# Performance work log

Hardware: AMD Instinct MI355X
Metric: run time of the kernel (lower is better)

Reference implementation:

```python
import jax, jax.numpy as jnp
import numpy as np

QUEST_DIM = 768
C, X, Y = 2048, 19, 19
B = 64

def setup_inputs() -> dict:
    key = jax.random.key(0)
    k1, k2, k3, k4 = jax.random.split(key, 4)
    text_fts = jax.random.normal(k1, (B, QUEST_DIM), dtype=jnp.float32)
    img_fts = jax.random.normal(k2, (B, C, X, Y), dtype=jnp.float32)
    # Linear params (PyTorch nn.Linear: y = x @ W.T + b)
    bound = 1.0 / np.sqrt(QUEST_DIM)
    W = jax.random.uniform(k3, (C, QUEST_DIM), minval=-bound, maxval=bound, dtype=jnp.float32)
    b = jax.random.uniform(k4, (C,), minval=-bound, maxval=bound, dtype=jnp.float32)
    return {"text_fts": text_fts, "img_fts": img_fts, "W": W, "b": b}

def reference(text_fts, img_fts, W, b):
    batch = text_fts.shape[0]
    q = text_fts @ W.T + b                      # [B, C]
    img_flat = img_fts.reshape(batch, C, X * Y) # [B, C, S]
    sims = jnp.einsum('bc,bcs->bs', q, img_flat)  # dot over channel dim
    weights = jax.nn.softmax(sims, axis=1)        # softmax over spatial locations
    final_ans = jnp.einsum('bcs,bs->bc', img_flat, weights)  # weighted pooling
    return final_ans
```

## Files before the change

### kernel.cpp

```cpp
#include <hip/hip_runtime.h>
#include <math.h>

#define Bsz  64
#define Cch  2048
#define Kdim 768
#define Ssp  361
#define CPB  16
#define REGF (CPB * Ssp)
#define NFULL 22
#define NTAIL 36

__device__ __forceinline__ void dma16(const float* g, float* l) {
    __builtin_amdgcn_global_load_lds(
        (const __attribute__((address_space(1))) void*)(g),
        (__attribute__((address_space(3))) void*)(l),
        16, 0, 0);
}

__device__ __forceinline__ void stage_slice(const float* region, float* lds,
                                            int wv, int lane) {
    for (int i = wv; i < NFULL + 1; i += 6) {
        if (i < NFULL || lane < NTAIL)
            dma16(region + i * 256 + lane * 4, lds + i * 256);
    }
    asm volatile("s_waitcnt vmcnt(0)" ::: "memory");
}

__global__ __launch_bounds__(256) void k_qgemm(
    const float* __restrict__ text, const float* __restrict__ W,
    const float* __restrict__ bias, float* __restrict__ qT)
{
    const int lane = threadIdx.x & 63;
    const int wv   = threadIdx.x >> 6;
    const int c0   = blockIdx.x * 8 + wv * 2;
    const int b0   = blockIdx.y * 8;

    const float4* wA = (const float4*)(W + (size_t)c0 * Kdim);
    const float4* wB = (const float4*)(W + (size_t)(c0 + 1) * Kdim);
    const float4 a0 = wA[lane*3+0], a1 = wA[lane*3+1], a2 = wA[lane*3+2];
    const float4 g0 = wB[lane*3+0], g1 = wB[lane*3+1], g2 = wB[lane*3+2];
    const float biasA = bias[c0], biasB = bias[c0 + 1];

    for (int b = b0; b < b0 + 8; b += 2) {
        const float4* tp = (const float4*)(text + (size_t)b * Kdim);
        const float4* up = (const float4*)(text + (size_t)(b + 1) * Kdim);
        const float4 t0 = tp[lane*3+0], t1 = tp[lane*3+1], t2 = tp[lane*3+2];
        const float4 u0 = up[lane*3+0], u1 = up[lane*3+1], u2 = up[lane*3+2];

        float r00 = a0.x*t0.x + a0.y*t0.y + a0.z*t0.z + a0.w*t0.w
                  + a1.x*t1.x + a1.y*t1.y + a1.z*t1.z + a1.w*t1.w
                  + a2.x*t2.x + a2.y*t2.y + a2.z*t2.z + a2.w*t2.w;
        float r10 = g0.x*t0.x + g0.y*t0.y + g0.z*t0.z + g0.w*t0.w
                  + g1.x*t1.x + g1.y*t1.y + g1.z*t1.z + g1.w*t1.w
                  + g2.x*t2.x + g2.y*t2.y + g2.z*t2.z + g2.w*t2.w;
        float r01 = a0.x*u0.x + a0.y*u0.y + a0.z*u0.z + a0.w*u0.w
                  + a1.x*u1.x + a1.y*u1.y + a1.z*u1.z + a1.w*u1.w
                  + a2.x*u2.x + a2.y*u2.y + a2.z*u2.z + a2.w*u2.w;
        float r11 = g0.x*u0.x + g0.y*u0.y + g0.z*u0.z + g0.w*u0.w
                  + g1.x*u1.x + g1.y*u1.y + g1.z*u1.z + g1.w*u1.w
                  + g2.x*u2.x + g2.y*u2.y + g2.z*u2.z + g2.w*u2.w;
        #pragma unroll
        for (int off = 32; off; off >>= 1) {
            r00 += __shfl_xor(r00, off);
            r10 += __shfl_xor(r10, off);
            r01 += __shfl_xor(r01, off);
            r11 += __shfl_xor(r11, off);
        }
        if (lane == 0) {
            qT[(size_t)c0 * Bsz + b]           = r00 + biasA;
            qT[(size_t)(c0 + 1) * Bsz + b]     = r10 + biasB;
            qT[(size_t)c0 * Bsz + b + 1]       = r01 + biasA;
            qT[(size_t)(c0 + 1) * Bsz + b + 1] = r11 + biasB;
        }
    }
}

__global__ __launch_bounds__(384) void k_sims(
    const float* __restrict__ img, const float* __restrict__ qT,
    float* __restrict__ sims_part)
{
    const int b  = blockIdx.x;
    const int cg = blockIdx.y;
    const int tid = threadIdx.x;
    const int lane = tid & 63;
    const int wv   = tid >> 6;

    __shared__ float lds[REGF];
    __shared__ float qL[CPB];

    if (tid < CPB) qL[tid] = qT[(size_t)(cg * CPB + tid) * Bsz + b];

    const float* region = img + ((size_t)b * Cch + (size_t)cg * CPB) * Ssp;
    stage_slice(region, lds, wv, lane);
    __syncthreads();

    if (tid < Ssp) {
        float acc = 0.f;
        #pragma unroll
        for (int c = 0; c < CPB; c++)
            acc += qL[c] * lds[c * Ssp + tid];
        sims_part[((size_t)b * 128 + cg) * Ssp + tid] = acc;
    }
}

__global__ __launch_bounds__(384) void k_wts(
    const float* __restrict__ sims_part, float* __restrict__ wts)
{
    const int b   = blockIdx.x;
    const int tid = threadIdx.x;
    const int lane = tid & 63;
    const int wv   = tid >> 6;

    __shared__ float red[6];

    float s0 = -1e30f;
    if (tid < Ssp) {
        const float* sp = sims_part + (size_t)b * 128 * Ssp + tid;
        float a = 0.f;
        for (int g0 = 0; g0 < 128; g0 += 16) {
            float v[16];
            #pragma unroll
            for (int j = 0; j < 16; j++) v[j] = sp[(size_t)(g0 + j) * Ssp];
            #pragma unroll
            for (int j = 0; j < 16; j++) a += v[j];
        }
        s0 = a;
    }

    float m = s0;
    #pragma unroll
    for (int off = 32; off; off >>= 1) m = fmaxf(m, __shfl_xor(m, off));
    if (lane == 0) red[wv] = m;
    __syncthreads();
    m = red[0];
    #pragma unroll
    for (int w = 1; w < 6; w++) m = fmaxf(m, red[w]);
    __syncthreads();

    const float e0 = (tid < Ssp) ? __expf(s0 - m) : 0.f;
    float l = e0;
    #pragma unroll
    for (int off = 32; off; off >>= 1) l += __shfl_xor(l, off);
    if (lane == 0) red[wv] = l;
    __syncthreads();
    l = red[0] + red[1] + red[2] + red[3] + red[4] + red[5];

    if (tid < Ssp)
        wts[(size_t)b * Ssp + tid] = e0 / l;
}

__global__ __launch_bounds__(384) void k_pool(
    const float* __restrict__ img, const float* __restrict__ wts,
    float* __restrict__ out)
{
    const int b   = blockIdx.x;
    const int cg  = blockIdx.y;
    const int tid = threadIdx.x;
    const int lane = tid & 63;
    const int wv   = tid >> 6;

    __shared__ float lds[REGF];
    __shared__ float wL[Ssp];
    __shared__ float partial[6 * CPB];

    if (tid < Ssp) wL[tid] = wts[(size_t)b * Ssp + tid];

    const float* region = img + ((size_t)b * Cch + (size_t)cg * CPB) * Ssp;
    stage_slice(region, lds, wv, lane);
    __syncthreads();

    const int c    = lane & 15;
    const int sl   = lane >> 4;
    const int s_lo = sl * 90 + (sl > 0 ? 1 : 0);
    const int s_hi = s_lo + (sl > 0 ? 90 : 91);

    float p = 0.f;
    for (int s = s_lo + wv; s < s_hi; s += 6)
        p += lds[c * Ssp + s] * wL[s];

    p += __shfl_xor(p, 16);
    p += __shfl_xor(p, 32);
    if (lane < CPB) partial[wv * CPB + lane] = p;
    __syncthreads();

    if (tid < CPB) {
        float r = partial[tid];
        #pragma unroll
        for (int w = 1; w < 6; w++) r += partial[w * CPB + tid];
        out[(size_t)b * Cch + (size_t)cg * CPB + tid] = r;
    }
}

extern "C" void kernel_launch(void* const* d_in, const int* in_sizes, int n_in,
                              void* d_out, int out_size, void* d_ws, size_t ws_size,
                              hipStream_t stream) {
    const float* text = (const float*)d_in[0];
    const float* img  = (const float*)d_in[1];
    const float* W    = (const float*)d_in[2];
    const float* bias = (const float*)d_in[3];
    float* out = (float*)d_out;

    float* qT        = (float*)d_ws;
    float* sims_part = qT + (size_t)Cch * Bsz;
    float* wts       = sims_part + (size_t)Bsz * 128 * Ssp;

    k_qgemm<<<dim3(256, 8),   256, 0, stream>>>(text, W, bias, qT);
    k_sims <<<dim3(Bsz, 128), 384, 0, stream>>>(img, qT, sims_part);
    k_wts  <<<dim3(Bsz),      384, 0, stream>>>(sims_part, wts);
    k_pool <<<dim3(Bsz, 128), 384, 0, stream>>>(img, wts, out);
}
```

Baseline: 316.7 us.

## Fuse all four stages into one persistent cooperative kernel with grid syncs

Replaces the four separate launches (query GEMM, partial sims, softmax, pooling) with a single cooperative persistent kernel that loops over work items and uses grid-wide syncs between phases. Grid size comes from the occupancy query and is rounded to a multiple of the batch size, so each block keeps one batch row of softmax weights in LDS. This removes kernel launch gaps and tail effects, at the cost of grid barrier overhead and fewer waves per block. If the cooperative launch fails, it falls back to the original four kernels.

```diff
diff --git a/kernel.cpp b/kernel.cpp
--- a/kernel.cpp
+++ b/kernel.cpp
@@ -1,5 +1,8 @@
 #include <hip/hip_runtime.h>
+#include <hip/hip_cooperative_groups.h>
 #include <math.h>
+
+namespace cg = cooperative_groups;
 
 #define Bsz  64
 #define Cch  2048
@@ -9,6 +12,8 @@
 #define REGF (CPB * Ssp)
 #define NFULL 22
 #define NTAIL 36
+#define NCG   (Cch / CPB)
+#define NSLICE (Bsz * NCG)
 
 __device__ __forceinline__ void dma16(const float* g, float* l) {
     __builtin_amdgcn_global_load_lds(
@@ -17,13 +22,179 @@
         16, 0, 0);
 }
 
+template <int NW>
 __device__ __forceinline__ void stage_slice(const float* region, float* lds,
                                             int wv, int lane) {
-    for (int i = wv; i < NFULL + 1; i += 6) {
+    for (int i = wv; i < NFULL + 1; i += NW) {
         if (i < NFULL || lane < NTAIL)
             dma16(region + i * 256 + lane * 4, lds + i * 256);
     }
     asm volatile("s_waitcnt vmcnt(0)" ::: "memory");
+}
+
+__global__ __launch_bounds__(256, 4) void k_fused(
+    const float* __restrict__ text, const float* __restrict__ img,
+    const float* __restrict__ W,    const float* __restrict__ bias,
+    float* __restrict__ qT, float* __restrict__ sims_part,
+    float* __restrict__ wts, float* __restrict__ out)
+{
+    const int tid  = threadIdx.x;
+    const int lane = tid & 63;
+    const int wv   = tid >> 6;
+    const int bid  = blockIdx.x;
+    const int nblk = gridDim.x;
+
+    __shared__ __align__(16) float lds[REGF];
+    __shared__ float aux[Ssp];
+    __shared__ float partial[256];
+
+    cg::grid_group grid = cg::this_grid();
+
+    for (int t = bid * 4 + wv; t < 8192; t += nblk * 4) {
+        const int c0 = (t & 1023) * 2;
+        const int b0 = (t >> 10) * 8;
+        const float4* wA = (const float4*)(W + (size_t)c0 * Kdim);
+        const float4* wB = (const float4*)(W + (size_t)(c0 + 1) * Kdim);
+        const float4 a0 = wA[lane*3+0], a1 = wA[lane*3+1], a2 = wA[lane*3+2];
+        const float4 g0 = wB[lane*3+0], g1 = wB[lane*3+1], g2 = wB[lane*3+2];
+        const float biasA = bias[c0], biasB = bias[c0 + 1];
+
+        for (int b = b0; b < b0 + 8; b += 2) {
+            const float4* tp = (const float4*)(text + (size_t)b * Kdim);
+            const float4* up = (const float4*)(text + (size_t)(b + 1) * Kdim);
+            const float4 t0 = tp[lane*3+0], t1 = tp[lane*3+1], t2 = tp[lane*3+2];
+            const float4 u0 = up[lane*3+0], u1 = up[lane*3+1], u2 = up[lane*3+2];
+
+            float r00 = a0.x*t0.x + a0.y*t0.y + a0.z*t0.z + a0.w*t0.w
+                      + a1.x*t1.x + a1.y*t1.y + a1.z*t1.z + a1.w*t1.w
+                      + a2.x*t2.x + a2.y*t2.y + a2.z*t2.z + a2.w*t2.w;
+            float r10 = g0.x*t0.x + g0.y*t0.y + g0.z*t0.z + g0.w*t0.w
+                      + g1.x*t1.x + g1.y*t1.y + g1.z*t1.z + g1.w*t1.w
+                      + g2.x*t2.x + g2.y*t2.y + g2.z*t2.z + g2.w*t2.w;
+            float r01 = a0.x*u0.x + a0.y*u0.y + a0.z*u0.z + a0.w*u0.w
+                      + a1.x*u1.x + a1.y*u1.y + a1.z*u1.z + a1.w*u1.w
+                      + a2.x*u2.x + a2.y*u2.y + a2.z*u2.z + a2.w*u2.w;
+            float r11 = g0.x*u0.x + g0.y*u0.y + g0.z*u0.z + g0.w*u0.w
+                      + g1.x*u1.x + g1.y*u1.y + g1.z*u1.z + g1.w*u1.w
+                      + g2.x*u2.x + g2.y*u2.y + g2.z*u2.z + g2.w*u2.w;
+            #pragma unroll
+            for (int off = 32; off; off >>= 1) {
+                r00 += __shfl_xor(r00, off);
+                r10 += __shfl_xor(r10, off);
+                r01 += __shfl_xor(r01, off);
+                r11 += __shfl_xor(r11, off);
+            }
+            if (lane == 0) {
+                qT[(size_t)c0 * Bsz + b]           = r00 + biasA;
+                qT[(size_t)(c0 + 1) * Bsz + b]     = r10 + biasB;
+                qT[(size_t)c0 * Bsz + b + 1]       = r01 + biasA;
+                qT[(size_t)(c0 + 1) * Bsz + b + 1] = r11 + biasB;
+            }
+        }
+    }
+
+    __threadfence();
+    grid.sync();
+    __threadfence();
+
+    for (int sl = bid; sl < NSLICE; sl += nblk) {
+        const int b   = sl & (Bsz - 1);
+        const int cgi = sl >> 6;
+        if (tid < CPB)
+            aux[tid] = qT[(size_t)(cgi * CPB + tid) * Bsz + b];
+        const float* region = img + ((size_t)b * Cch + (size_t)cgi * CPB) * Ssp;
+        stage_slice<4>(region, lds, wv, lane);
+        __syncthreads();
+        for (int s = tid; s < Ssp; s += 256) {
+            float acc = 0.f;
+            #pragma unroll
+            for (int c = 0; c < CPB; c++)
+                acc += aux[c] * lds[c * Ssp + s];
+            sims_part[((size_t)b * NCG + cgi) * Ssp + s] = acc;
+        }
+        __syncthreads();
+    }
+
+    __threadfence();
+    grid.sync();
+    __threadfence();
+
+    if (bid < Bsz) {
+        const int b = bid;
+        const float* sp = sims_part + (size_t)b * NCG * Ssp;
+        float sa, sb = -1e30f;
+        {
+            float a = 0.f;
+            for (int g0 = 0; g0 < NCG; g0 += 16) {
+                float v[16];
+                #pragma unroll
+                for (int j = 0; j < 16; j++) v[j] = sp[(size_t)(g0 + j) * Ssp + tid];
+                #pragma unroll
+                for (int j = 0; j < 16; j++) a += v[j];
+            }
+            sa = a;
+        }
+        if (tid < Ssp - 256) {
+            float a = 0.f;
+            for (int g0 = 0; g0 < NCG; g0 += 16) {
+                float v[16];
+                #pragma unroll
+                for (int j = 0; j < 16; j++) v[j] = sp[(size_t)(g0 + j) * Ssp + tid + 256];
+                #pragma unroll
+                for (int j = 0; j < 16; j++) a += v[j];
+            }
+            sb = a;
+        }
+        float m = fmaxf(sa, sb);
+        #pragma unroll
+        for (int off = 32; off; off >>= 1) m = fmaxf(m, __shfl_xor(m, off));
+        if (lane == 0) partial[wv] = m;
+        __syncthreads();
+        m = fmaxf(fmaxf(partial[0], partial[1]), fmaxf(partial[2], partial[3]));
+        __syncthreads();
+        const float ea = __expf(sa - m);
+        const float eb = (tid < Ssp - 256) ? __expf(sb - m) : 0.f;
+        float l = ea + eb;
+        #pragma unroll
+        for (int off = 32; off; off >>= 1) l += __shfl_xor(l, off);
+        if (lane == 0) partial[wv] = l;
+        __syncthreads();
+        l = partial[0] + partial[1] + partial[2] + partial[3];
+        wts[(size_t)b * Ssp + tid] = ea / l;
+        if (tid < Ssp - 256) wts[(size_t)b * Ssp + tid + 256] = eb / l;
+    }
+
+    __threadfence();
+    grid.sync();
+    __threadfence();
+
+    {
+        const int b = bid & (Bsz - 1);
+        for (int s = tid; s < Ssp; s += 256)
+            aux[s] = wts[(size_t)b * Ssp + s];
+    }
+    __syncthreads();
+    for (int sl = bid; sl < NSLICE; sl += nblk) {
+        const int b   = sl & (Bsz - 1);
+        const int cgi = sl >> 6;
+        const float* region = img + ((size_t)b * Cch + (size_t)cgi * CPB) * Ssp;
+        stage_slice<4>(region, lds, wv, lane);
+        __syncthreads();
+        const int c = tid & 15;
+        const int g = tid >> 4;
+        float p = 0.f;
+        for (int s = g; s < Ssp; s += 16)
+            p += lds[c * Ssp + s] * aux[s];
+        partial[tid] = p;
+        __syncthreads();
+        if (tid < CPB) {
+            float r = 0.f;
+            #pragma unroll
+            for (int gg = 0; gg < 16; gg++) r += partial[gg * 16 + tid];
+            out[(size_t)b * Cch + (size_t)cgi * CPB + tid] = r;
+        }
+        __syncthreads();
+    }
 }
 
 __global__ __launch_bounds__(256) void k_qgemm(
@@ -80,7 +251,7 @@
     float* __restrict__ sims_part)
 {
     const int b  = blockIdx.x;
-    const int cg = blockIdx.y;
+    const int cgi = blockIdx.y;
     const int tid = threadIdx.x;
     const int lane = tid & 63;
     const int wv   = tid >> 6;
@@ -88,10 +259,10 @@
     __shared__ float lds[REGF];
     __shared__ float qL[CPB];
 
-    if (tid < CPB) qL[tid] = qT[(size_t)(cg * CPB + tid) * Bsz + b];
-
-    const float* region = img + ((size_t)b * Cch + (size_t)cg * CPB) * Ssp;
-    stage_slice(region, lds, wv, lane);
+    if (tid < CPB) qL[tid] = qT[(size_t)(cgi * CPB + tid) * Bsz + b];
+
+    const float* region = img + ((size_t)b * Cch + (size_t)cgi * CPB) * Ssp;
+    stage_slice<6>(region, lds, wv, lane);
     __syncthreads();
 
     if (tid < Ssp) {
@@ -99,7 +270,7 @@
         #pragma unroll
         for (int c = 0; c < CPB; c++)
             acc += qL[c] * lds[c * Ssp + tid];
-        sims_part[((size_t)b * 128 + cg) * Ssp + tid] = acc;
+        sims_part[((size_t)b * NCG + cgi) * Ssp + tid] = acc;
     }
 }
 
@@ -115,9 +286,9 @@
 
     float s0 = -1e30f;
     if (tid < Ssp) {
-        const float* sp = sims_part + (size_t)b * 128 * Ssp + tid;
+        const float* sp = sims_part + (size_t)b * NCG * Ssp + tid;
         float a = 0.f;
-        for (int g0 = 0; g0 < 128; g0 += 16) {
+        for (int g0 = 0; g0 < NCG; g0 += 16) {
             float v[16];
             #pragma unroll
             for (int j = 0; j < 16; j++) v[j] = sp[(size_t)(g0 + j) * Ssp];
@@ -154,7 +325,7 @@
     float* __restrict__ out)
 {
     const int b   = blockIdx.x;
-    const int cg  = blockIdx.y;
+    const int cgi = blockIdx.y;
     const int tid = threadIdx.x;
     const int lane = tid & 63;
     const int wv   = tid >> 6;
@@ -165,8 +336,8 @@
 
     if (tid < Ssp) wL[tid] = wts[(size_t)b * Ssp + tid];
 
-    const float* region = img + ((size_t)b * Cch + (size_t)cg * CPB) * Ssp;
-    stage_slice(region, lds, wv, lane);
+    const float* region = img + ((size_t)b * Cch + (size_t)cgi * CPB) * Ssp;
+    stage_slice<6>(region, lds, wv, lane);
     __syncthreads();
 
     const int c    = lane & 15;
@@ -187,7 +358,7 @@
         float r = partial[tid];
         #pragma unroll
         for (int w = 1; w < 6; w++) r += partial[w * CPB + tid];
-        out[(size_t)b * Cch + (size_t)cg * CPB + tid] = r;
+        out[(size_t)b * Cch + (size_t)cgi * CPB + tid] = r;
     }
 }
 
@@ -202,10 +373,49 @@
 
     float* qT        = (float*)d_ws;
     float* sims_part = qT + (size_t)Cch * Bsz;
-    float* wts       = sims_part + (size_t)Bsz * 128 * Ssp;
-
-    k_qgemm<<<dim3(256, 8),   256, 0, stream>>>(text, W, bias, qT);
-    k_sims <<<dim3(Bsz, 128), 384, 0, stream>>>(img, qT, sims_part);
-    k_wts  <<<dim3(Bsz),      384, 0, stream>>>(sims_part, wts);
-    k_pool <<<dim3(Bsz, 128), 384, 0, stream>>>(img, wts, out);
-}
+    float* wts       = sims_part + (size_t)Bsz * NCG * Ssp;
+
+    static int mode = 0;
+    static int nblk = 1024;
+    if (mode == 0) {
+        int bpc = 0;
+        if (hipOccupancyMaxActiveBlocksPerMultiprocessor(
+                &bpc, reinterpret_cast<const void*>(&k_fused), 256, 0) != hipSuccess
+            || bpc < 1)
+            bpc = 2;
+        int cus = 256;
+        hipDeviceProp_t prop;
+        int dev = 0;
+        if (hipGetDevice(&dev) == hipSuccess &&
+            hipGetDeviceProperties(&prop, dev) == hipSuccess &&
+            prop.multiProcessorCount > 0)
+            cus = prop.multiProcessorCount;
+        long long nb = (long long)bpc * cus;
+        if (nb > 2048) nb = 2048;
+        nb -= nb % 64;
+        if (nb < 64) nb = 64;
+        nblk = (int)nb;
+        mode = 1;
+    }
+
+    bool done = false;
+    if (mode != 2) {
+        void* args[8] = {(void*)&text, (void*)&img, (void*)&W, (void*)&bias,
+                         (void*)&qT, (void*)&sims_part, (void*)&wts, (void*)&out};
+        hipError_t e = hipLaunchCooperativeKernel(
+            reinterpret_cast<const void*>(&k_fused),
+            dim3(nblk), dim3(256), args, 0, stream);
+        if (e == hipSuccess) {
+            done = true;
+        } else {
+            mode = 2;
+            (void)hipGetLastError();
+        }
+    }
+    if (!done) {
+        k_qgemm<<<dim3(256, 8),   256, 0, stream>>>(text, W, bias, qT);
+        k_sims <<<dim3(Bsz, NCG), 384, 0, stream>>>(img, qT, sims_part);
+        k_wts  <<<dim3(Bsz),      384, 0, stream>>>(sims_part, wts);
+        k_pool <<<dim3(Bsz, NCG), 384, 0, stream>>>(img, wts, out);
+    }
+}
```

After: 711.4 us. 2.25x slower.

## Restructure pooling kernel to read image directly with per-wave channel rows

Applied to the files above, without the earlier changes.

The pooling kernel no longer stages a 16-channel slice into LDS through global_load_lds DMA. Each block now covers 128 channels and each wave covers 32 of them, four rows at a time. Every lane loads spatial elements straight from global memory, multiplies them by weights held in registers, and reduces across the wave with shuffles. This removes the LDS staging, the barrier wait and the cross-wave partial reduction, and cuts the grid from 8192 to 1024 blocks. The cost is lower parallelism, and the row loads are unaligned and coalesced only per row, with a tail that is partly masked.

```diff
diff --git a/kernel.cpp b/kernel.cpp
--- a/kernel.cpp
+++ b/kernel.cpp
@@ -9,6 +9,7 @@
 #define REGF (CPB * Ssp)
 #define NFULL 22
 #define NTAIL 36
+#define NCG   (Cch / CPB)
 
 __device__ __forceinline__ void dma16(const float* g, float* l) {
     __builtin_amdgcn_global_load_lds(
@@ -99,7 +100,7 @@
         #pragma unroll
         for (int c = 0; c < CPB; c++)
             acc += qL[c] * lds[c * Ssp + tid];
-        sims_part[((size_t)b * 128 + cg) * Ssp + tid] = acc;
+        sims_part[((size_t)b * NCG + cg) * Ssp + tid] = acc;
     }
 }
 
@@ -115,7 +116,7 @@
 
     float s0 = -1e30f;
     if (tid < Ssp) {
-        const float* sp = sims_part + (size_t)b * 128 * Ssp + tid;
+        const float* sp = sims_part + (size_t)b * NCG * Ssp + tid;
         float a = 0.f;
         for (int g0 = 0; g0 < 128; g0 += 16) {
             float v[16];
@@ -149,45 +150,62 @@
         wts[(size_t)b * Ssp + tid] = e0 / l;
 }
 
-__global__ __launch_bounds__(384) void k_pool(
+__global__ __launch_bounds__(256) void k_pool(
     const float* __restrict__ img, const float* __restrict__ wts,
     float* __restrict__ out)
 {
-    const int b   = blockIdx.x;
-    const int cg  = blockIdx.y;
-    const int tid = threadIdx.x;
+    const int b    = blockIdx.x;
+    const int cg   = blockIdx.y;
+    const int tid  = threadIdx.x;
     const int lane = tid & 63;
     const int wv   = tid >> 6;
 
-    __shared__ float lds[REGF];
     __shared__ float wL[Ssp];
-    __shared__ float partial[6 * CPB];
-
-    if (tid < Ssp) wL[tid] = wts[(size_t)b * Ssp + tid];
-
-    const float* region = img + ((size_t)b * Cch + (size_t)cg * CPB) * Ssp;
-    stage_slice(region, lds, wv, lane);
-    __syncthreads();
-
-    const int c    = lane & 15;
-    const int sl   = lane >> 4;
-    const int s_lo = sl * 90 + (sl > 0 ? 1 : 0);
-    const int s_hi = s_lo + (sl > 0 ? 90 : 91);
-
-    float p = 0.f;
-    for (int s = s_lo + wv; s < s_hi; s += 6)
-        p += lds[c * Ssp + s] * wL[s];
-
-    p += __shfl_xor(p, 16);
-    p += __shfl_xor(p, 32);
-    if (lane < CPB) partial[wv * CPB + lane] = p;
-    __syncthreads();
-
-    if (tid < CPB) {
-        float r = partial[tid];
-        #pragma unroll
-        for (int w = 1; w < 6; w++) r += partial[w * CPB + tid];
-        out[(size_t)b * Cch + (size_t)cg * CPB + tid] = r;
+    for (int s = tid; s < Ssp; s += 256)
+        wL[s] = wts[(size_t)b * Ssp + s];
+    __syncthreads();
+
+    float wreg[6];
+    #pragma unroll
+    for (int k = 0; k < 6; k++) {
+        const int s = lane + 64 * k;
+        wreg[k] = (s < Ssp) ? wL[s] : 0.f;
+    }
+
+    const float* base = img + ((size_t)b * Cch + (size_t)cg * 128) * Ssp;
+    const int c0 = wv * 32;
+
+    for (int i = 0; i < 32; i += 4) {
+        const float* r0 = base + (size_t)(c0 + i + 0) * Ssp;
+        const float* r1 = base + (size_t)(c0 + i + 1) * Ssp;
+        const float* r2 = base + (size_t)(c0 + i + 2) * Ssp;
+        const float* r3 = base + (size_t)(c0 + i + 3) * Ssp;
+
+        float a0 = 0.f, a1 = 0.f, a2 = 0.f, a3 = 0.f;
+        #pragma unroll
+        for (int k = 0; k < 6; k++) {
+            const int s = lane + 64 * k;
+            const bool ok = (s < Ssp);
+            const float v0 = ok ? r0[s] : 0.f;
+            const float v1 = ok ? r1[s] : 0.f;
+            const float v2 = ok ? r2[s] : 0.f;
+            const float v3 = ok ? r3[s] : 0.f;
+            a0 += v0 * wreg[k];
+            a1 += v1 * wreg[k];
+            a2 += v2 * wreg[k];
+            a3 += v3 * wreg[k];
+        }
+        #pragma unroll
+        for (int off = 32; off; off >>= 1) {
+            a0 += __shfl_xor(a0, off);
+            a1 += __shfl_xor(a1, off);
+            a2 += __shfl_xor(a2, off);
+            a3 += __shfl_xor(a3, off);
+        }
+        if (lane == 0) {
+            float* o = out + (size_t)b * Cch + (size_t)cg * 128 + c0 + i;
+            o[0] = a0; o[1] = a1; o[2] = a2; o[3] = a3;
+        }
     }
 }
 
@@ -202,10 +220,10 @@
 
     float* qT        = (float*)d_ws;
     float* sims_part = qT + (size_t)Cch * Bsz;
-    float* wts       = sims_part + (size_t)Bsz * 128 * Ssp;
+    float* wts       = sims_part + (size_t)Bsz * NCG * Ssp;
 
     k_qgemm<<<dim3(256, 8),   256, 0, stream>>>(text, W, bias, qT);
-    k_sims <<<dim3(Bsz, 128), 384, 0, stream>>>(img, qT, sims_part);
+    k_sims <<<dim3(Bsz, NCG), 384, 0, stream>>>(img, qT, sims_part);
     k_wts  <<<dim3(Bsz),      384, 0, stream>>>(sims_part, wts);
-    k_pool <<<dim3(Bsz, 128), 384, 0, stream>>>(img, wts, out);
-}
+    k_pool <<<dim3(Bsz, 16),  256, 0, stream>>>(img, wts, out);
+}
```

Measured after the change: 319.0 us. About the same (+0.8%).
